# Kernel optimization log

Hardware: AMD Instinct MI355X
Metric: run time of the kernel (lower is better)

The kernel has to match this reference:

```python
import jax, jax.numpy as jnp
import numpy as np

EMB_DIM = 1024
H = 16
HEAD_DIM = EMB_DIM // H
B = 2
S = 2048  # enc and dec seq len
LN_EPS = 1e-5


def setup_inputs() -> dict:
    key = jax.random.key(0)
    ks = jax.random.split(key, 8)
    scale_in = 1.0 / np.sqrt(EMB_DIM)
    scale_o = 1.0 / np.sqrt(H * HEAD_DIM)
    return {
        "enc_out": jax.random.normal(ks[0], (B, S, EMB_DIM), jnp.float32),
        "dec_out": jax.random.normal(ks[1], (B, S, EMB_DIM), jnp.float32),
        # stacked per-head projections, equivalent to h separate Linear(emb_dim, head_dim, bias=False)
        "Wq": jax.random.uniform(ks[2], (H, EMB_DIM, HEAD_DIM), jnp.float32, -scale_in, scale_in),
        "Wk": jax.random.uniform(ks[3], (H, EMB_DIM, HEAD_DIM), jnp.float32, -scale_in, scale_in),
        "Wv": jax.random.uniform(ks[4], (H, EMB_DIM, HEAD_DIM), jnp.float32, -scale_in, scale_in),
        "Wo": jax.random.uniform(ks[5], (H * HEAD_DIM, EMB_DIM), jnp.float32, -scale_o, scale_o),
        "gamma": jnp.ones((EMB_DIM,), jnp.float32),
        "beta": jnp.zeros((EMB_DIM,), jnp.float32),
    }


def reference(enc_out, dec_out, Wq, Wk, Wv, Wo, gamma, beta):
    d = Wq.shape[-1]
    # per-head projections, batched over heads (same math as the Python loop)
    q = jnp.einsum('bse,hed->bhsd', dec_out, Wq)   # queries from decoder
    k = jnp.einsum('bte,hed->bhtd', enc_out, Wk)   # keys from encoder
    v = jnp.einsum('bte,hed->bhtd', enc_out, Wv)   # values from encoder
    scores = jnp.einsum('bhsd,bhtd->bhst', q, k) / jnp.sqrt(jnp.asarray(d, q.dtype))
    att = jax.nn.softmax(scores, axis=-1)
    ctx = jnp.einsum('bhst,bhtd->bhsd', att, v)
    b, h, s, hd = ctx.shape
    ctx = ctx.transpose(0, 2, 1, 3).reshape(b, s, h * hd)  # concat heads along feature dim
    transformed = ctx @ Wo  # dropout is identity in eval mode
    x = dec_out + transformed
    mu = jnp.mean(x, axis=-1, keepdims=True)
    var = jnp.mean(jnp.square(x - mu), axis=-1, keepdims=True)
    return (x - mu) * jax.lax.rsqrt(var + LN_EPS) * gamma + beta
```

## Files before the change

### kernel.cpp

```cpp
#include <hip/hip_runtime.h>
#include <hip/hip_bf16.h>

#define EMB   1024
#define NH    16
#define HD    64
#define SEQ   2048
#define SA    72

typedef __attribute__((ext_vector_type(8))) short          bf16x8;
typedef __attribute__((ext_vector_type(8))) unsigned short us8;
typedef __attribute__((ext_vector_type(4))) float          f32x4;

__device__ __forceinline__ float u2f(unsigned short u) {
    return __uint_as_float(((unsigned)u) << 16);
}
__device__ __forceinline__ unsigned short f2u(float f) {
    __hip_bfloat16 b = __float2bfloat16(f);
    return *reinterpret_cast<unsigned short*>(&b);
}
__device__ __forceinline__ bool detect_bf16(const void* gamma) {
    return ((const unsigned short*)gamma)[0] == 0x3F80;
}
__device__ __forceinline__ f32x4 fzero() {
    f32x4 v; v.x = v.y = v.z = v.w = 0.f; return v;
}
__device__ __forceinline__ void ld16f(const void* p, size_t idx, bool isbf, float* o) {
    if (isbf) {
        const unsigned short* b = (const unsigned short*)p + idx;
        us8 v0 = *(const us8*)b, v1 = *(const us8*)(b + 8);
        #pragma unroll
        for (int i = 0; i < 8; ++i) { o[i] = u2f(v0[i]); o[8 + i] = u2f(v1[i]); }
    } else {
        const float* f = (const float*)p + idx;
        #pragma unroll
        for (int i = 0; i < 4; ++i) {
            float4 v = *(const float4*)(f + 4 * i);
            o[4*i] = v.x; o[4*i+1] = v.y; o[4*i+2] = v.z; o[4*i+3] = v.w;
        }
    }
}
__device__ __forceinline__ float4 ld4(const void* p, size_t idx, bool isbf) {
    if (isbf) {
        ushort4 t = *reinterpret_cast<const ushort4*>((const unsigned short*)p + idx);
        return make_float4(u2f(t.x), u2f(t.y), u2f(t.z), u2f(t.w));
    }
    return *reinterpret_cast<const float4*>((const float*)p + idx);
}
__device__ __forceinline__ us8 pk8(const float* s) {
    us8 v;
    #pragma unroll
    for (int i = 0; i < 8; ++i) v[i] = f2u(s[i]);
    return v;
}
__device__ __forceinline__ f32x4 mfma16(bf16x8 a, bf16x8 b, f32x4 c) {
    return __builtin_amdgcn_mfma_f32_16x16x32_bf16(a, b, c, 0, 0, 0);
}
__device__ __forceinline__ bf16x8 mk8(unsigned w0, unsigned w1, unsigned w2, unsigned w3) {
    union { unsigned u[4]; bf16x8 v; } x;
    x.u[0] = w0; x.u[1] = w1; x.u[2] = w2; x.u[3] = w3;
    return x.v;
}
__device__ __forceinline__ float fexp2(float x) {
    return __builtin_amdgcn_exp2f(x);
}
__device__ __forceinline__ unsigned cvtpk(float lo, float hi) {
    unsigned r;
    asm("v_cvt_pk_bf16_f32 %0, %1, %2" : "=v"(r) : "v"(lo), "v"(hi));
    return r;
}
__device__ __forceinline__ void gl_lds16(const unsigned short* g, unsigned short* l) {
    __builtin_amdgcn_global_load_lds(
        (const __attribute__((address_space(1))) void*)g,
        (__attribute__((address_space(3))) void*)l,
        16, 0, 0);
}

#define QSCALE 0.18033688f

__global__ __launch_bounds__(256) void prep_kernel(
    const void* __restrict__ dec, const void* __restrict__ enc,
    const void* __restrict__ Wq, const void* __restrict__ Wk,
    const void* __restrict__ Wv, const void* __restrict__ Wo,
    const void* __restrict__ gamma,
    unsigned short* __restrict__ xb,
    unsigned short* __restrict__ wt,
    unsigned short* __restrict__ wot)
{
    const bool isbf = detect_bf16(gamma);
    const int blk = blockIdx.x;
    __shared__ unsigned short T[64][SA];

    if (blk < 2048) {
        const size_t HALF = (size_t)4096 * 1024;
        size_t idx = ((size_t)blk * 256 + threadIdx.x) * 16;
        const void* src; size_t off;
        if (idx < HALF) { src = dec; off = idx; } else { src = enc; off = idx - HALF; }
        float buf[16];
        ld16f(src, off, isbf, buf);
        *(us8*)&xb[idx]     = pk8(buf);
        *(us8*)&xb[idx + 8] = pk8(buf + 8);
    } else if (blk < 2816) {
        const int local = blk - 2048;
        const int which = local >> 8, h = (local >> 4) & 15, e0 = (local & 15) * 64;
        const void* W = (which == 0) ? Wq : (which == 1 ? Wk : Wv);
        const int sr = threadIdx.x >> 2, sc = (threadIdx.x & 3) * 16;

        float buf[16];
        ld16f(W, ((size_t)h * EMB + e0 + sr) * HD + sc, isbf, buf);
        #pragma unroll
        for (int i = 0; i < 16; ++i) T[sc + i][sr] = f2u(buf[i]);
        __syncthreads();
        us8 v0 = *(const us8*)&T[sr][sc];
        us8 v1 = *(const us8*)&T[sr][sc + 8];
        size_t o = (((size_t)which * NH + h) * HD + sr) * EMB + e0 + sc;
        *(us8*)&wt[o] = v0;
        *(us8*)&wt[o + 8] = v1;
    } else {
        const int local = blk - 2816;
        const int n0 = (local & 15) * 64, k0 = (local >> 4) * 64;
        const int sr = threadIdx.x >> 2, sc = (threadIdx.x & 3) * 16;

        float buf[16];
        ld16f(Wo, (size_t)(k0 + sr) * EMB + n0 + sc, isbf, buf);
        #pragma unroll
        for (int i = 0; i < 16; ++i) T[sc + i][sr] = f2u(buf[i]);
        __syncthreads();
        us8 v0 = *(const us8*)&T[sr][sc];
        us8 v1 = *(const us8*)&T[sr][sc + 8];
        size_t o = (size_t)(n0 + sr) * EMB + k0 + sc;
        *(us8*)&wot[o] = v0;
        *(us8*)&wot[o + 8] = v1;
    }
}

__global__ __launch_bounds__(256) void qkv_kernel(
    const unsigned short* __restrict__ xb,
    const unsigned short* __restrict__ wt,
    unsigned short* __restrict__ qo, unsigned short* __restrict__ ko,
    unsigned short* __restrict__ vt)
{
    const int id = blockIdx.x;
    const int xcd = id & 7, sl = id >> 3;
    const int m_t = (xcd & 3) * 8 + (sl & 7);
    const int n_t = (xcd >> 2) * 12 + (sl >> 3);
    const int m0 = m_t * 128, n0g = n_t * 128;
    const int which = n0g >> 10;
    const int nloc = n0g & 1023;
    const unsigned short* X = xb + ((which == 0) ? (size_t)0 : (size_t)4096 * 1024);

    __shared__ unsigned short smem[17408];
    unsigned short* const ldsA = smem;
    unsigned short* const ldsB = smem + 8192;

    const int tid = threadIdx.x, wv = tid >> 6, lane = tid & 63;
    const int lq = lane >> 4, lm = lane & 15;
    const int mw = (wv & 1) * 64, nw = (wv >> 1) * 64;

    const unsigned short* Wb = wt + (size_t)(which * 1024 + nloc) * EMB;

    const int seg0 = wv * 4;
    const int srow = lane >> 3;
    const int su   = (lane & 7) ^ srow;
    const unsigned short* aP[4];
    const unsigned short* bP[4];
    #pragma unroll
    for (int q = 0; q < 4; ++q) {
        const int s = seg0 + q;
        aP[q] = X  + (size_t)(m0 + 8 * s + srow) * EMB + su * 8;
        bP[q] = Wb + (size_t)(8 * s + srow) * EMB + su * 8;
    }

    f32x4 acc[4][4];
    #pragma unroll
    for (int i = 0; i < 4; ++i)
        #pragma unroll
        for (int j = 0; j < 4; ++j) acc[i][j] = fzero();

    const int xa = lm & 7;

    for (int k0 = 0; k0 < EMB; k0 += 64) {
        #pragma unroll
        for (int q = 0; q < 4; ++q) {
            gl_lds16(aP[q] + k0, ldsA + (seg0 + q) * 512);
            gl_lds16(bP[q] + k0, ldsB + (seg0 + q) * 512);
        }
        asm volatile("s_waitcnt vmcnt(0)" ::: "memory");
        __syncthreads();

        #pragma unroll
        for (int st = 0; st < 2; ++st) {
            const int u = (st * 4 + lq) ^ xa;
            bf16x8 af[4], bq[4];
            #pragma unroll
            for (int i = 0; i < 4; ++i)
                af[i] = *(const bf16x8*)(ldsA + (mw + i * 16 + lm) * 64 + u * 8);
            #pragma unroll
            for (int j = 0; j < 4; ++j)
                bq[j] = *(const bf16x8*)(ldsB + (nw + j * 16 + lm) * 64 + u * 8);
            #pragma unroll
            for (int i = 0; i < 4; ++i)
                #pragma unroll
                for (int j = 0; j < 4; ++j)
                    acc[i][j] = mfma16(af[i], bq[j], acc[i][j]);
        }
        __syncthreads();
    }

    const int b = m0 >> 11, s0 = m0 & (SEQ - 1);
    const float osc = (which == 0) ? QSCALE : 1.0f;
    if (which != 2) {
        unsigned short* Y = which ? ko : qo;
        #pragma unroll
        for (int i = 0; i < 4; ++i)
            #pragma unroll
            for (int j = 0; j < 4; ++j)
                #pragma unroll
                for (int r = 0; r < 4; ++r) {
                    int m = mw + i * 16 + lq * 4 + r;
                    int n = nloc + nw + j * 16 + lm;
                    int h = n >> 6, d = n & 63;
                    Y[(((size_t)b * NH + h) * SEQ + s0 + m) * HD + d] = f2u(acc[i][j][r] * osc);
                }
    } else {
        __syncthreads();
        unsigned short* vbuf = smem;
        #pragma unroll
        for (int i = 0; i < 4; ++i)
            #pragma unroll
            for (int j = 0; j < 4; ++j) {
                ushort4 p;
                p.x = f2u(acc[i][j][0]); p.y = f2u(acc[i][j][1]);
                p.z = f2u(acc[i][j][2]); p.w = f2u(acc[i][j][3]);
                *(ushort4*)&vbuf[(size_t)(nw + j * 16 + lm) * 136 + mw + i * 16 + lq * 4] = p;
            }
        __syncthreads();
        const int dd = tid >> 1, cc = (tid & 1) * 64;
        const int n = nloc + dd, h = n >> 6, d = n & 63;
        size_t o = (((size_t)b * NH + h) * HD + d) * SEQ + s0 + cc;
        #pragma unroll
        for (int jj = 0; jj < 8; ++jj)
            *(us8*)&vt[o + 8 * jj] = *(const us8*)&vbuf[(size_t)dd * 136 + cc + 8 * jj];
    }
}

__global__ __launch_bounds__(128) void attn_kernel(
    const unsigned short* __restrict__ qg,
    const unsigned short* __restrict__ kg,
    const unsigned short* __restrict__ vtg,
    unsigned short* __restrict__ ctx)
{
    __shared__ unsigned short Ks[2][4096];
    __shared__ unsigned short Vt[2][4096];

    const int tid = threadIdx.x, wv = tid >> 6, lane = tid & 63;
    const int lq = lane >> 4, lm = lane & 15;
    const int bh = blockIdx.x, q0 = blockIdx.y * 64;
    const unsigned short* Kg = kg + (size_t)bh * SEQ * HD;
    const unsigned short* Vg = vtg + (size_t)bh * HD * SEQ;

    const int srow = lane >> 3;
    const int su   = (lane & 7) ^ srow;
    const unsigned short* kSp[4];
    const unsigned short* vSp[4];
    #pragma unroll
    for (int j = 0; j < 4; ++j) {
        const int seg = wv + 2 * j;
        kSp[j] = Kg + (size_t)(8 * seg + srow) * HD  + su * 8;
        vSp[j] = Vg + (size_t)(8 * seg + srow) * SEQ + su * 8;
    }

    bf16x8 qf[2][2];
    #pragma unroll
    for (int s = 0; s < 2; ++s)
        #pragma unroll
        for (int st = 0; st < 2; ++st)
            qf[s][st] = *(const bf16x8*)(qg + (size_t)bh * SEQ * HD
                          + (size_t)(q0 + wv * 32 + s * 16 + lm) * HD + st * 32 + lq * 8);

    bf16x8 onesf;
    #pragma unroll
    for (int i = 0; i < 8; ++i) onesf[i] = (short)0x3F80;

    f32x4 Of[2][4], lacc[2];
    #pragma unroll
    for (int s = 0; s < 2; ++s) {
        lacc[s] = fzero();
        #pragma unroll
        for (int t = 0; t < 4; ++t) Of[s][t] = fzero();
    }

    const int xa = lm & 7;

    #pragma unroll
    for (int j = 0; j < 4; ++j) {
        gl_lds16(kSp[j], &Ks[0][(wv + 2 * j) * 512]);
        gl_lds16(vSp[j], &Vt[0][(wv + 2 * j) * 512]);
    }

    for (int it = 0; it < SEQ / 64; ++it) {
        const int cur = it & 1;
        if (it + 1 < SEQ / 64) {
            const size_t ko = (size_t)(it + 1) * 64 * HD;
            const int    vo = (it + 1) * 64;
            #pragma unroll
            for (int j = 0; j < 4; ++j) {
                gl_lds16(kSp[j] + ko, &Ks[cur ^ 1][(wv + 2 * j) * 512]);
                gl_lds16(vSp[j] + vo, &Vt[cur ^ 1][(wv + 2 * j) * 512]);
            }
            asm volatile("s_waitcnt vmcnt(8)" ::: "memory");
        } else {
            asm volatile("s_waitcnt vmcnt(0)" ::: "memory");
        }
        __syncthreads();

        f32x4 sf[2][4];
        #pragma unroll
        for (int s = 0; s < 2; ++s)
            #pragma unroll
            for (int t = 0; t < 4; ++t) sf[s][t] = fzero();
        __builtin_amdgcn_s_setprio(1);
        #pragma unroll
        for (int st = 0; st < 2; ++st) {
            const int u = (st * 4 + lq) ^ xa;
            #pragma unroll
            for (int tt = 0; tt < 4; ++tt) {
                bf16x8 kf = *(const bf16x8*)&Ks[cur][(lm + 16 * tt) * 64 + u * 8];
                sf[0][tt] = mfma16(kf, qf[0][st], sf[0][tt]);
                sf[1][tt] = mfma16(kf, qf[1][st], sf[1][tt]);
            }
        }
        __builtin_amdgcn_s_setprio(0);

        unsigned pw[2][4][2];
        #pragma unroll
        for (int s = 0; s < 2; ++s)
            #pragma unroll
            for (int tt = 0; tt < 4; ++tt) {
                pw[s][tt][0] = cvtpk(fexp2(sf[s][tt][0]), fexp2(sf[s][tt][1]));
                pw[s][tt][1] = cvtpk(fexp2(sf[s][tt][2]), fexp2(sf[s][tt][3]));
            }
        #pragma unroll
        for (int s = 0; s < 2; ++s)
            #pragma unroll
            for (int a = 0; a < 2; ++a)
                #pragma unroll
                for (int c = 0; c < 2; ++c)
                    asm("v_permlane32_swap_b32 %0, %1"
                        : "+v"(pw[s][2 * a][c]), "+v"(pw[s][2 * a + 1][c]));
        #pragma unroll
        for (int s = 0; s < 2; ++s)
            #pragma unroll
            for (int a = 0; a < 2; ++a)
                #pragma unroll
                for (int c = 0; c < 2; ++c)
                    asm("v_permlane16_swap_b32 %0, %1"
                        : "+v"(pw[s][2 * a][c]), "+v"(pw[s][2 * a + 1][c]));

        __builtin_amdgcn_s_setprio(1);
        #pragma unroll
        for (int st = 0; st < 2; ++st) {
            const int u = (st * 4 + lq) ^ xa;
            bf16x8 pf0 = mk8(pw[0][2 * st][0], pw[0][2 * st][1],
                             pw[0][2 * st + 1][0], pw[0][2 * st + 1][1]);
            bf16x8 pf1 = mk8(pw[1][2 * st][0], pw[1][2 * st][1],
                             pw[1][2 * st + 1][0], pw[1][2 * st + 1][1]);
            #pragma unroll
            for (int t = 0; t < 4; ++t) {
                bf16x8 vf = *(const bf16x8*)&Vt[cur][(lm + 16 * t) * 64 + u * 8];
                Of[0][t] = mfma16(pf0, vf, Of[0][t]);
                Of[1][t] = mfma16(pf1, vf, Of[1][t]);
            }
            lacc[0] = mfma16(pf0, onesf, lacc[0]);
            lacc[1] = mfma16(pf1, onesf, lacc[1]);
        }
        __builtin_amdgcn_s_setprio(0);
        __syncthreads();
    }

    const int b = bh >> 4, h = bh & 15;
    #pragma unroll
    for (int s = 0; s < 2; ++s)
        #pragma unroll
        for (int r = 0; r < 4; ++r) {
            float inv = 1.0f / lacc[s][r];
            int srow2 = q0 + wv * 32 + s * 16 + lq * 4 + r;
            #pragma unroll
            for (int t = 0; t < 4; ++t) {
                int d = lm + 16 * t;
                ctx[((size_t)b * SEQ + srow2) * EMB + h * HD + d] = f2u(Of[s][t][r] * inv);
            }
        }
}

__global__ __launch_bounds__(256) void oproj_kernel(
    const unsigned short* __restrict__ ctx,
    const unsigned short* __restrict__ wot,
    const unsigned short* __restrict__ xdec,
    unsigned short* __restrict__ x)
{
    const int id = blockIdx.x;
    const int xcd = id & 7, sl = id >> 3;
    const int m0 = (xcd * 8 + (sl & 7)) * 64;
    const int n0 = (sl >> 3) * 128;

    __shared__ unsigned short smem[12288];
    unsigned short* const ldsA = smem;
    unsigned short* const ldsB = smem + 4096;

    const int tid = threadIdx.x, wv = tid >> 6, lane = tid & 63;
    const int lq = lane >> 4, lm = lane & 15;
    const int mw = (wv & 1) * 32, nw = (wv >> 1) * 64;

    const int srow = lane >> 3;
    const int su   = (lane & 7) ^ srow;
    const unsigned short* aP[2];
    const unsigned short* bP[4];
    #pragma unroll
    for (int q = 0; q < 2; ++q)
        aP[q] = ctx + (size_t)(m0 + 8 * (wv + 4 * q) + srow) * EMB + su * 8;
    #pragma unroll
    for (int q = 0; q < 4; ++q)
        bP[q] = wot + (size_t)(n0 + 8 * (wv + 4 * q) + srow) * EMB + su * 8;

    f32x4 acc[2][4];
    #pragma unroll
    for (int i = 0; i < 2; ++i)
        #pragma unroll
        for (int j = 0; j < 4; ++j) acc[i][j] = fzero();

    const int xa = lm & 7;

    for (int k0 = 0; k0 < EMB; k0 += 64) {
        #pragma unroll
        for (int q = 0; q < 2; ++q)
            gl_lds16(aP[q] + k0, ldsA + (wv + 4 * q) * 512);
        #pragma unroll
        for (int q = 0; q < 4; ++q)
            gl_lds16(bP[q] + k0, ldsB + (wv + 4 * q) * 512);
        asm volatile("s_waitcnt vmcnt(0)" ::: "memory");
        __syncthreads();

        #pragma unroll
        for (int st = 0; st < 2; ++st) {
            const int u = (st * 4 + lq) ^ xa;
            bf16x8 af[2], bq[4];
            #pragma unroll
            for (int i = 0; i < 2; ++i)
                af[i] = *(const bf16x8*)(ldsA + (mw + i * 16 + lm) * 64 + u * 8);
            #pragma unroll
            for (int j = 0; j < 4; ++j)
                bq[j] = *(const bf16x8*)(ldsB + (nw + j * 16 + lm) * 64 + u * 8);
            #pragma unroll
            for (int i = 0; i < 2; ++i)
                #pragma unroll
                for (int j = 0; j < 4; ++j)
                    acc[i][j] = mfma16(af[i], bq[j], acc[i][j]);
        }
        __syncthreads();
    }

    #pragma unroll
    for (int i = 0; i < 2; ++i)
        #pragma unroll
        for (int j = 0; j < 4; ++j)
            #pragma unroll
            for (int r = 0; r < 4; ++r) {
                int m = m0 + mw + i * 16 + lq * 4 + r;
                int n = n0 + nw + j * 16 + lm;
                size_t o = (size_t)m * EMB + n;
                x[o] = f2u(acc[i][j][r] + u2f(xdec[o]));
            }
}

__global__ __launch_bounds__(256) void ln_kernel(
    const unsigned short* __restrict__ x,
    const void* __restrict__ gamma,
    const void* __restrict__ beta,
    void* __restrict__ out)
{
    const bool isbf = detect_bf16(gamma);
    const int row = blockIdx.x;
    const int tid = threadIdx.x;
    const unsigned short* xr = x + (size_t)row * EMB;

    ushort4 t = *reinterpret_cast<const ushort4*>(&xr[tid * 4]);
    float4 xv = make_float4(u2f(t.x), u2f(t.y), u2f(t.z), u2f(t.w));
    float s1 = xv.x + xv.y + xv.z + xv.w;
    float s2 = xv.x * xv.x + xv.y * xv.y + xv.z * xv.z + xv.w * xv.w;

    #pragma unroll
    for (int off = 32; off > 0; off >>= 1) {
        s1 += __shfl_down(s1, off);
        s2 += __shfl_down(s2, off);
    }
    __shared__ float w1[4], w2[4];
    const int wid = tid >> 6, lane = tid & 63;
    if (lane == 0) { w1[wid] = s1; w2[wid] = s2; }
    __syncthreads();
    s1 = w1[0] + w1[1] + w1[2] + w1[3];
    s2 = w2[0] + w2[1] + w2[2] + w2[3];

    const float mu  = s1 * (1.0f / EMB);
    const float var = s2 * (1.0f / EMB) - mu * mu;
    const float rs  = rsqrtf(var + 1e-5f);

    float4 gv = ld4(gamma, (size_t)tid * 4, isbf);
    float4 bv = ld4(beta,  (size_t)tid * 4, isbf);
    float4 r;
    r.x = (xv.x - mu) * rs * gv.x + bv.x;
    r.y = (xv.y - mu) * rs * gv.y + bv.y;
    r.z = (xv.z - mu) * rs * gv.z + bv.z;
    r.w = (xv.w - mu) * rs * gv.w + bv.w;

    size_t o = (size_t)row * EMB + tid * 4;
    if (isbf) {
        ushort4 w;
        w.x = f2u(r.x); w.y = f2u(r.y); w.z = f2u(r.z); w.w = f2u(r.w);
        *reinterpret_cast<ushort4*>((unsigned short*)out + o) = w;
    } else {
        *reinterpret_cast<float4*>((float*)out + o) = r;
    }
}

extern "C" void kernel_launch(void* const* d_in, const int* in_sizes, int n_in,
                              void* d_out, int out_size, void* d_ws, size_t ws_size,
                              hipStream_t stream)
{
    const void* enc   = d_in[0];
    const void* dec   = d_in[1];
    const void* Wq    = d_in[2];
    const void* Wk    = d_in[3];
    const void* Wv    = d_in[4];
    const void* Wo    = d_in[5];
    const void* gamma = d_in[6];
    const void* beta  = d_in[7];

    char* w = (char*)d_ws;
    unsigned short* qws  = (unsigned short*)(w);
    unsigned short* kws  = (unsigned short*)(w + (size_t)8  * 1024 * 1024);
    unsigned short* vtws = (unsigned short*)(w + (size_t)16 * 1024 * 1024);
    unsigned short* wtws = (unsigned short*)(w + (size_t)24 * 1024 * 1024);
    unsigned short* wotw = (unsigned short*)(w + (size_t)30 * 1024 * 1024);
    unsigned short* xws  = (unsigned short*)(w);
    unsigned short* xbuf = (unsigned short*)d_out;
    unsigned short* cws  = (unsigned short*)d_out + (size_t)4096 * 1024;

    prep_kernel  <<<3072,          256, 0, stream>>>(dec, enc, Wq, Wk, Wv, Wo,
                                                     gamma, xbuf, wtws, wotw);
    qkv_kernel   <<<768,           256, 0, stream>>>(xbuf, wtws, qws, kws, vtws);
    attn_kernel  <<<dim3(32, 32),  128, 0, stream>>>(qws, kws, vtws, cws);
    oproj_kernel <<<512,           256, 0, stream>>>(cws, wotw, xbuf, xws);
    ln_kernel    <<<4096,          256, 0, stream>>>(xws, gamma, beta, d_out);
}
```

Baseline: 226.0 us.

## Double-buffer QKV projection GEMM with K-tile 32 and async prefetch

The QKV projection GEMM main loop now uses two LDS buffers with a K step of 32 instead of a single buffer with K step 64. The next tile's global-to-LDS loads are issued before computing on the current tile, and the wait uses vmcnt(4) so the loads overlap the MFMAs. This hides global load latency, but halves the work per barrier and needs a new XOR swizzle for the 32-wide rows.

```diff
diff --git a/kernel.cpp b/kernel.cpp
--- a/kernel.cpp
+++ b/kernel.cpp
@@ -158,16 +158,15 @@
 
     const unsigned short* Wb = wt + (size_t)(which * 1024 + nloc) * EMB;
 
-    const int seg0 = wv * 4;
-    const int srow = lane >> 3;
-    const int su   = (lane & 7) ^ srow;
-    const unsigned short* aP[4];
-    const unsigned short* bP[4];
-    #pragma unroll
-    for (int q = 0; q < 4; ++q) {
-        const int s = seg0 + q;
-        aP[q] = X  + (size_t)(m0 + 8 * s + srow) * EMB + su * 8;
-        bP[q] = Wb + (size_t)(8 * s + srow) * EMB + su * 8;
+    const int sr2 = lane >> 2;
+    const int su2 = (lane & 3) ^ ((lane >> 3) & 3);
+    const unsigned short* aP[2];
+    const unsigned short* bP[2];
+    #pragma unroll
+    for (int q = 0; q < 2; ++q) {
+        const int seg = wv + 4 * q;
+        aP[q] = X  + (size_t)(m0 + 16 * seg + sr2) * EMB + su2 * 8;
+        bP[q] = Wb + (size_t)(16 * seg + sr2) * EMB + su2 * 8;
     }
 
     f32x4 acc[4][4];
@@ -176,33 +175,44 @@
         #pragma unroll
         for (int j = 0; j < 4; ++j) acc[i][j] = fzero();
 
-    const int xa = lm & 7;
-
-    for (int k0 = 0; k0 < EMB; k0 += 64) {
-        #pragma unroll
-        for (int q = 0; q < 4; ++q) {
-            gl_lds16(aP[q] + k0, ldsA + (seg0 + q) * 512);
-            gl_lds16(bP[q] + k0, ldsB + (seg0 + q) * 512);
-        }
-        asm volatile("s_waitcnt vmcnt(0)" ::: "memory");
-        __syncthreads();
-
-        #pragma unroll
-        for (int st = 0; st < 2; ++st) {
-            const int u = (st * 4 + lq) ^ xa;
-            bf16x8 af[4], bq[4];
-            #pragma unroll
-            for (int i = 0; i < 4; ++i)
-                af[i] = *(const bf16x8*)(ldsA + (mw + i * 16 + lm) * 64 + u * 8);
+    const int u = lq ^ ((lm >> 1) & 3);
+
+    #pragma unroll
+    for (int q = 0; q < 2; ++q) {
+        gl_lds16(aP[q], ldsA + (wv + 4 * q) * 512);
+        gl_lds16(bP[q], ldsB + (wv + 4 * q) * 512);
+    }
+
+    for (int it = 0; it < EMB / 32; ++it) {
+        const int cur = it & 1;
+        if (it + 1 < EMB / 32) {
+            const int kn = (it + 1) * 32;
+            const int nb = (cur ^ 1) * 4096;
+            #pragma unroll
+            for (int q = 0; q < 2; ++q) {
+                gl_lds16(aP[q] + kn, ldsA + nb + (wv + 4 * q) * 512);
+                gl_lds16(bP[q] + kn, ldsB + nb + (wv + 4 * q) * 512);
+            }
+            asm volatile("s_waitcnt vmcnt(4)" ::: "memory");
+        } else {
+            asm volatile("s_waitcnt vmcnt(0)" ::: "memory");
+        }
+        __syncthreads();
+
+        const unsigned short* Ac = ldsA + cur * 4096;
+        const unsigned short* Bc = ldsB + cur * 4096;
+        bf16x8 af[4], bq[4];
+        #pragma unroll
+        for (int i = 0; i < 4; ++i)
+            af[i] = *(const bf16x8*)(Ac + (mw + i * 16 + lm) * 32 + u * 8);
+        #pragma unroll
+        for (int j = 0; j < 4; ++j)
+            bq[j] = *(const bf16x8*)(Bc + (nw + j * 16 + lm) * 32 + u * 8);
+        #pragma unroll
+        for (int i = 0; i < 4; ++i)
             #pragma unroll
             for (int j = 0; j < 4; ++j)
-                bq[j] = *(const bf16x8*)(ldsB + (nw + j * 16 + lm) * 64 + u * 8);
-            #pragma unroll
-            for (int i = 0; i < 4; ++i)
-                #pragma unroll
-                for (int j = 0; j < 4; ++j)
-                    acc[i][j] = mfma16(af[i], bq[j], acc[i][j]);
-        }
+                acc[i][j] = mfma16(af[i], bq[j], acc[i][j]);
         __syncthreads();
     }
 
```

After: 221.4 us. 2.0% less time.
